# Optimization experiments

Hardware: AMD Instinct MI355X
Metric: run time of the kernel (lower is better)

The kernel has to match this reference:

```python
import jax, jax.numpy as jnp
import numpy as np

B, C, H, W = 8, 256, 64, 64
CI = 128  # inter_channels = in_channels // reduction

def _conv1x1(x, w, b):
    # x: [b, c, h, w], w: [o, c], b: [o]
    return jnp.einsum('bchw,oc->bohw', x, w) + b[None, :, None, None]

def setup_inputs() -> dict:
    key = jax.random.key(0)
    ks = jax.random.split(key, 5)
    s_in = 1.0 / np.sqrt(C)
    s_ci = 1.0 / np.sqrt(CI)
    return {
        'x': jax.random.normal(ks[0], (B, C, H, W), jnp.float32),
        'w_g': jax.random.normal(ks[1], (CI, C), jnp.float32) * s_in,
        'b_g': jnp.zeros((CI,), jnp.float32),
        'w_theta': jax.random.normal(ks[2], (CI, C), jnp.float32) * s_in,
        'b_theta': jnp.zeros((CI,), jnp.float32),
        'w_phi': jax.random.normal(ks[3], (CI, C), jnp.float32) * s_in,
        'b_phi': jnp.zeros((CI,), jnp.float32),
        'w_out': jax.random.normal(ks[4], (C, CI), jnp.float32) * s_ci,
        'b_out': jnp.zeros((C,), jnp.float32),
    }

def reference(x, w_g, b_g, w_theta, b_theta, w_phi, b_phi, w_out, b_out):
    n, c, h, w = x.shape
    N = h * w
    g_x = _conv1x1(x, w_g, b_g).reshape(n, CI, N).transpose(0, 2, 1)        # [b, N, ci]
    theta_x = _conv1x1(x, w_theta, b_theta).reshape(n, CI, N).transpose(0, 2, 1)  # [b, N, ci]
    phi_x = _conv1x1(x, w_phi, b_phi).reshape(n, CI, N)                     # [b, ci, N]
    pw = jnp.einsum('bnc,bcm->bnm', theta_x, phi_x)                         # [b, N, N]
    # Faithful to source: divides by ci**(-0.5) == multiplies by sqrt(ci)
    pw = pw / (jnp.asarray(CI, x.dtype) ** -0.5)
    pw = jax.nn.softmax(pw, axis=-1)
    y = jnp.einsum('bnm,bmc->bnc', pw, g_x)                                 # [b, N, ci]
    y = y.transpose(0, 2, 1).reshape(n, CI, h, w)
    return x + _conv1x1(y, w_out, b_out)
```

## Files before the change

kernel.cpp:

```cpp
#include <hip/hip_runtime.h>
#include <hip/hip_bf16.h>
#include <stdint.h>
#include <stddef.h>


typedef __bf16 bf16;
typedef __attribute__((ext_vector_type(8))) __bf16 bf16x8;
typedef __attribute__((ext_vector_type(4))) __bf16 bf16x4;
typedef __attribute__((ext_vector_type(4))) float  f32x4;
typedef __attribute__((ext_vector_type(4))) int    i32x4;

#define MFMA16(a, b, c) __builtin_amdgcn_mfma_f32_16x16x32_bf16((a), (b), (c), 0, 0, 0)

constexpr int NB  = 8;
constexpr int NC  = 256;
constexpr int NN  = 4096;
constexpr int NCI = 128;
constexpr size_t NEL = (size_t)NB * NN * NCI;
constexpr int PBATCH = NN * NCI;

#define QSCALE (11.313708498984761f * 1.4426950408889634f)


__global__ __launch_bounds__(256) void k_proj3(
    const float* __restrict__ x,
    const float* __restrict__ wt, const float* __restrict__ bt,
    const float* __restrict__ wp, const float* __restrict__ bp,
    const float* __restrict__ wg, const float* __restrict__ bg,
    const float* __restrict__ wo, bf16* __restrict__ wob,
    bf16* __restrict__ qh, bf16* __restrict__ ql,
    bf16* __restrict__ kh, bf16* __restrict__ kl,
    bf16* __restrict__ vv)
{
    const int nt  = blockIdx.x;
    const int b   = blockIdx.y;
    const int tid = threadIdx.x;
    const int wv  = tid >> 6;
    const int ln  = tid & 63;
    const int lg  = ln >> 4;
    const int lq  = ln & 15;

    if (wob != nullptr && tid < 16) {
        int idx = (b * 64 + nt) * 64 + tid * 4;
        f32x4 w4 = *(const f32x4*)(wo + idx);
        bf16x4 o4;
#pragma unroll
        for (int e = 0; e < 4; ++e) o4[e] = (bf16)w4[e];
        *(bf16x4*)(wob + idx) = o4;
    }

    __shared__ char lds[49152];
    char* Ah = lds;
    char* Al = lds + 8192;
    char* Wh = lds + 16384;
    char* Wl = lds + 32768;

    f32x4 acc[3][8];
#pragma unroll
    for (int pj = 0; pj < 3; ++pj)
#pragma unroll
        for (int j = 0; j < 8; ++j) acc[pj][j] = f32x4{0.f, 0.f, 0.f, 0.f};

    const int n0 = nt * 64;

    for (int c0 = 0; c0 < NC; c0 += 64) {
        __syncthreads();
#pragma unroll
        for (int p = 0; p < 4; ++p) {
            int cc = p * 16 + (tid >> 4);
            int nn = (tid & 15) * 4;
            f32x4 xv = *(const f32x4*)(x + ((size_t)b * NC + (c0 + cc)) * NN + n0 + nn);
#pragma unroll
            for (int e = 0; e < 4; ++e) {
                float f = xv[e];
                bf16 hh = (bf16)f;
                int row = nn + e;
                int off = (row * 128 + cc * 2) ^ ((row & 7) << 4);
                *(bf16*)(Ah + off) = hh;
                *(bf16*)(Al + off) = (bf16)(f - (float)hh);
            }
        }

#pragma unroll
        for (int pj = 0; pj < 3; ++pj) {
            const float* W = (pj == 0) ? wt : (pj == 1) ? wp : wg;
            const bool split = (pj != 2);
            if (pj != 0) __syncthreads();
#pragma unroll
            for (int p = 0; p < 8; ++p) {
                int i  = p * 16 + (tid >> 4);
                int c4 = (tid & 15) * 4;
                f32x4 w4 = *(const f32x4*)(W + (size_t)i * NC + c0 + c4);
                bf16x4 hv, lv;
#pragma unroll
                for (int e = 0; e < 4; ++e) {
                    bf16 hh = (bf16)w4[e];
                    hv[e] = hh;
                    lv[e] = (bf16)(w4[e] - (float)hh);
                }
                int off = (i * 128 + c4 * 2) ^ ((i & 7) << 4);
                *(bf16x4*)(Wh + off) = hv;
                if (split) *(bf16x4*)(Wl + off) = lv;
            }
            __syncthreads();
#pragma unroll
            for (int kk = 0; kk < 2; ++kk) {
                int row  = wv * 16 + lq;
                int koff = kk * 64 + lg * 16;
                int aoff = (row * 128 + koff) ^ ((row & 7) << 4);
                bf16x8 ah = *(const bf16x8*)(Ah + aoff);
                bf16x8 al = *(const bf16x8*)(Al + aoff);
#pragma unroll
                for (int j = 0; j < 8; ++j) {
                    int ir   = j * 16 + lq;
                    int woff = (ir * 128 + koff) ^ ((ir & 7) << 4);
                    bf16x8 bh = *(const bf16x8*)(Wh + woff);
                    acc[pj][j] = MFMA16(ah, bh, acc[pj][j]);
                    if (split) {
                        bf16x8 bl = *(const bf16x8*)(Wl + woff);
                        acc[pj][j] = MFMA16(ah, bl, acc[pj][j]);
                        acc[pj][j] = MFMA16(al, bh, acc[pj][j]);
                    }
                }
            }
        }
    }

#pragma unroll
    for (int j = 0; j < 8; ++j) {
        int i = j * 16 + lq;
        float bvt = bt[i];
        float bvp = bp[i];
#pragma unroll
        for (int r = 0; r < 4; ++r) {
            int q = n0 + wv * 16 + lg * 4 + r;
            size_t off = ((size_t)b * NN + q) * NCI + i;
            float vt2 = (acc[0][j][r] + bvt) * QSCALE;
            bf16 th = (bf16)vt2;
            qh[off] = th; ql[off] = (bf16)(vt2 - (float)th);
            float vp2 = acc[1][j][r] + bvp;
            bf16 phh = (bf16)vp2;
            kh[off] = phh; kl[off] = (bf16)(vp2 - (float)phh);
        }
    }

    __syncthreads();
    char* T = lds;
#pragma unroll
    for (int j = 0; j < 8; ++j) {
        int i = j * 16 + lq;
        float bv2 = bg[i];
#pragma unroll
        for (int r = 0; r < 4; ++r) {
            int nl = wv * 16 + lg * 4 + r;
            int off = (i * 128 + nl * 2) ^ ((i & 7) << 4);
            *(bf16*)(T + off) = (bf16)(acc[2][j][r] + bv2);
        }
    }
    __syncthreads();
#pragma unroll
    for (int p = 0; p < 4; ++p) {
        int i  = p * 32 + (tid >> 3);
        int sl = tid & 7;
        i32x4 tv = *(const i32x4*)(T + ((i * 128 + sl * 16) ^ ((i & 7) << 4)));
        size_t off = (size_t)b * PBATCH
                   + (size_t)((((nt * 8 + (i >> 4)) * 2 + (sl >> 2)) * 64
                               + (sl & 3) * 16 + (i & 15)) * 8);
        *(i32x4*)(vv + off) = tv;
    }
}

__global__ __launch_bounds__(128, 2) void k_attn_sp(
    const bf16* __restrict__ qh, const bf16* __restrict__ ql,
    const bf16* __restrict__ kh, const bf16* __restrict__ kl,
    const bf16* __restrict__ vf,
    bf16* __restrict__ p0, bf16* __restrict__ p1, float* __restrict__ ml)
{
    const int bid = blockIdx.x;
    const int b   = bid & 7;
    const int rs  = bid >> 3;
    const int qt  = rs & 63;
    const int h   = rs >> 6;
    const int tid = threadIdx.x;
    const int wv  = tid >> 6;
    const int ln  = tid & 63;
    const int lg  = ln >> 4;
    const int lq  = ln & 15;
    const int n0  = qt * 64;
    const int mb0 = h * 2048;
    bf16* ph = h ? p1 : p0;

    __shared__ __attribute__((aligned(16))) char lds[36864];
    char* P = lds + 32768 + wv * 2048;

    const int smm = tid >> 4;
    const int ssl = tid & 15;

    bf16x8 qhf[2][4], qlf[2][4];
#pragma unroll
    for (int q2 = 0; q2 < 2; ++q2) {
        int qrow = n0 + wv * 32 + q2 * 16 + lq;
        const bf16* bh = qh + ((size_t)b * NN + qrow) * NCI;
        const bf16* bl = ql + ((size_t)b * NN + qrow) * NCI;
#pragma unroll
        for (int kk = 0; kk < 4; ++kk) {
            qhf[q2][kk] = *(const bf16x8*)(bh + kk * 32 + lg * 8);
            qlf[q2][kk] = *(const bf16x8*)(bl + kk * 32 + lg * 8);
        }
    }

    f32x4 o[2][8];
#pragma unroll
    for (int q2 = 0; q2 < 2; ++q2)
#pragma unroll
        for (int j = 0; j < 8; ++j) o[q2][j] = f32x4{0.f, 0.f, 0.f, 0.f};
    float mrun[2] = {-1e30f, -1e30f};
    float lrun[2] = {0.f, 0.f};

    const bf16* vb = vf + (size_t)b * PBATCH + (size_t)ln * 8;

    {
#pragma unroll
        for (int p = 0; p < 4; ++p) {
            int mm = p * 8 + smm;
            size_t g = ((size_t)b * NN + mb0 + mm) * NCI + ssl * 8;
            i32x4 hv = *(const i32x4*)(kh + g);
            i32x4 lv = *(const i32x4*)(kl + g);
            int off = (mm * 256 + ssl * 16) ^ ((mm & 7) << 4);
            *(i32x4*)(lds + off) = hv;
            *(i32x4*)(lds + 8192 + off) = lv;
        }
    }
    __syncthreads();

    for (int t = 0; t < 64; ++t) {
        const int cur = t & 1;
        char* KHc = lds + cur * 16384;
        char* KLc = KHc + 8192;
        char* KHn = lds + (cur ^ 1) * 16384;
        char* KLn = KHn + 8192;
        const bool pre = (t < 63);

        i32x4 rkh[4], rkl[4];
        if (pre) {
#pragma unroll
            for (int p = 0; p < 4; ++p) {
                size_t g = ((size_t)b * NN + mb0 + (t + 1) * 32 + p * 8 + smm) * NCI + ssl * 8;
                rkh[p] = *(const i32x4*)(kh + g);
                rkl[p] = *(const i32x4*)(kl + g);
            }
        }
        __builtin_amdgcn_sched_barrier(0);

        f32x4 s[2][2];
        __builtin_amdgcn_s_setprio(1);
#pragma unroll
        for (int jm = 0; jm < 2; ++jm) {
            s[jm][0] = f32x4{0.f, 0.f, 0.f, 0.f};
            s[jm][1] = f32x4{0.f, 0.f, 0.f, 0.f};
            const int mrow = jm * 16 + lq;
            const int sw = (mrow & 7) << 4;
#pragma unroll
            for (int kk = 0; kk < 4; ++kk) {
                int aoff = (mrow * 256 + kk * 64 + lg * 16) ^ sw;
                bf16x8 ah = *(const bf16x8*)(KHc + aoff);
                bf16x8 al = *(const bf16x8*)(KLc + aoff);
                s[jm][0] = MFMA16(ah, qhf[0][kk], s[jm][0]);
                s[jm][1] = MFMA16(ah, qhf[1][kk], s[jm][1]);
                s[jm][0] = MFMA16(al, qhf[0][kk], s[jm][0]);
                s[jm][1] = MFMA16(al, qhf[1][kk], s[jm][1]);
                s[jm][0] = MFMA16(ah, qlf[0][kk], s[jm][0]);
                s[jm][1] = MFMA16(ah, qlf[1][kk], s[jm][1]);
            }
        }
        __builtin_amdgcn_s_setprio(0);

        bf16x8 bv[8];
        {
            const bf16* vp = vb + (size_t)(h * 32 + (t >> 1)) * 8192;
#pragma unroll
            for (int j = 0; j < 8; ++j)
                bv[j] = *(const bf16x8*)(vp + (j * 2 + (t & 1)) * 512);
        }
        __builtin_amdgcn_sched_barrier(0);

        if (pre) {
#pragma unroll
            for (int p = 0; p < 4; ++p) {
                int mm = p * 8 + smm;
                int off = (mm * 256 + ssl * 16) ^ ((mm & 7) << 4);
                *(i32x4*)(KHn + off) = rkh[p];
                *(i32x4*)(KLn + off) = rkl[p];
            }
        }

        float tm[2];
        tm[0] = s[0][0][0];
        tm[1] = s[0][1][0];
#pragma unroll
        for (int jm = 0; jm < 2; ++jm)
#pragma unroll
            for (int r = 0; r < 4; ++r) {
                tm[0] = fmaxf(tm[0], s[jm][0][r]);
                tm[1] = fmaxf(tm[1], s[jm][1][r]);
            }
#pragma unroll
        for (int q2 = 0; q2 < 2; ++q2) {
            tm[q2] = fmaxf(tm[q2], __shfl_xor(tm[q2], 16));
            tm[q2] = fmaxf(tm[q2], __shfl_xor(tm[q2], 32));
        }

        bool grow = (tm[0] > mrun[0] + 8.f) || (tm[1] > mrun[1] + 8.f);
        if (__any(grow)) {
            float alpha[2];
#pragma unroll
            for (int q2 = 0; q2 < 2; ++q2) {
                float mnew = fmaxf(mrun[q2], tm[q2]);
                alpha[q2] = exp2f(mrun[q2] - mnew);
                mrun[q2] = mnew;
                lrun[q2] *= alpha[q2];
            }
            float av0[4], av1[4];
#pragma unroll
            for (int r = 0; r < 4; ++r) {
                av0[r] = __shfl(alpha[0], lg * 4 + r);
                av1[r] = __shfl(alpha[1], lg * 4 + r);
            }
#pragma unroll
            for (int j = 0; j < 8; ++j)
#pragma unroll
                for (int r = 0; r < 4; ++r) {
                    o[0][j][r] *= av0[r];
                    o[1][j][r] *= av1[r];
                }
        }

        float psum[2] = {0.f, 0.f};
#pragma unroll
        for (int jm = 0; jm < 2; ++jm)
#pragma unroll
            for (int q2 = 0; q2 < 2; ++q2) {
                bf16x4 pk;
#pragma unroll
                for (int r = 0; r < 4; ++r) {
                    float e2 = exp2f(s[jm][q2][r] - mrun[q2]);
                    psum[q2] += e2;
                    pk[r] = (bf16)e2;
                }
                int row = q2 * 16 + lq;
                int off = (row * 64 + (jm * 16 + lg * 4) * 2) ^ ((row & 7) << 4);
                *(bf16x4*)(P + off) = pk;
            }
#pragma unroll
        for (int q2 = 0; q2 < 2; ++q2) {
            psum[q2] += __shfl_xor(psum[q2], 16);
            psum[q2] += __shfl_xor(psum[q2], 32);
            lrun[q2] += psum[q2];
        }

        bf16x8 pa[2];
#pragma unroll
        for (int q2 = 0; q2 < 2; ++q2) {
            int row = q2 * 16 + lq;
            pa[q2] = *(const bf16x8*)(P + ((row * 64 + lg * 16) ^ ((row & 7) << 4)));
        }
        __builtin_amdgcn_s_setprio(1);
#pragma unroll
        for (int j = 0; j < 8; ++j) {
            o[0][j] = MFMA16(pa[0], bv[j], o[0][j]);
            o[1][j] = MFMA16(pa[1], bv[j], o[1][j]);
        }
        __builtin_amdgcn_s_setprio(0);

        __syncthreads();
    }

    float rl0[4], rl1[4];
#pragma unroll
    for (int r = 0; r < 4; ++r) {
        rl0[r] = 1.f / __shfl(lrun[0], lg * 4 + r);
        rl1[r] = 1.f / __shfl(lrun[1], lg * 4 + r);
    }
#pragma unroll
    for (int j = 0; j < 8; ++j) {
        int d = j * 16 + lq;
#pragma unroll
        for (int r = 0; r < 4; ++r) {
            int q0 = n0 + wv * 32 + lg * 4 + r;
            ph[((size_t)b * NN + q0) * NCI + d]      = (bf16)(o[0][j][r] * rl0[r]);
            ph[((size_t)b * NN + q0 + 16) * NCI + d] = (bf16)(o[1][j][r] * rl1[r]);
        }
    }
    if (lg == 0) {
#pragma unroll
        for (int q2 = 0; q2 < 2; ++q2) {
            int row = n0 + wv * 32 + q2 * 16 + lq;
            size_t base = ((size_t)b * NN + row) * 4 + h * 2;
            ml[base]     = mrun[q2];
            ml[base + 1] = lrun[q2];
        }
    }
}

__global__ __launch_bounds__(256) void k_out(
    const bf16* __restrict__ p0, const bf16* __restrict__ p1,
    const float* __restrict__ ml, const float* __restrict__ x,
    const float* __restrict__ w_out, const bf16* __restrict__ wob,
    const float* __restrict__ b_out, float* __restrict__ out)
{
    const int nt  = blockIdx.x;
    const int b   = blockIdx.y;
    const int tid = threadIdx.x;
    const int wv  = tid >> 6;
    const int ln  = tid & 63;
    const int lg  = ln >> 4;
    const int lq  = ln & 15;
    const int n0  = nt * 64;

    __shared__ char Y[16384];
#pragma unroll
    for (int p = 0; p < 4; ++p) {
        int nn = p * 16 + (tid >> 4);
        int d0 = (tid & 15) * 8;
        size_t row = (size_t)b * NN + n0 + nn;
        f32x4 q = *(const f32x4*)(ml + row * 4);
        float M  = fmaxf(q[0], q[2]);
        float w0 = exp2f(q[0] - M) * q[1];
        float w1 = exp2f(q[2] - M) * q[3];
        float inv = 1.f / (w0 + w1);
        w0 *= inv; w1 *= inv;
        size_t off = row * NCI + d0;
        bf16x8 a = *(const bf16x8*)(p0 + off);
        bf16x8 c = *(const bf16x8*)(p1 + off);
        bf16x8 rr;
#pragma unroll
        for (int e = 0; e < 8; ++e)
            rr[e] = (bf16)(w0 * (float)a[e] + w1 * (float)c[e]);
        *(bf16x8*)(Y + ((nn * 256 + d0 * 2) ^ ((nn & 7) << 4))) = rr;
    }
    __syncthreads();

    bf16x8 af[4];
    {
        int row = wv * 16 + lq;
#pragma unroll
        for (int kk = 0; kk < 4; ++kk) {
            int koff = kk * 64 + lg * 16;
            af[kk] = *(const bf16x8*)(Y + ((row * 256 + koff) ^ ((row & 7) << 4)));
        }
    }

    f32x4 acc[16];
#pragma unroll
    for (int j = 0; j < 16; ++j) acc[j] = f32x4{0.f, 0.f, 0.f, 0.f};

    if (wob != nullptr) {
#pragma unroll
        for (int j = 0; j < 16; ++j) {
            int c = j * 16 + lq;
#pragma unroll
            for (int kk = 0; kk < 4; ++kk) {
                int i0 = kk * 32 + lg * 8;
                bf16x8 bw = *(const bf16x8*)(wob + (size_t)c * NCI + i0);
                acc[j] = MFMA16(af[kk], bw, acc[j]);
            }
        }
    } else {
#pragma unroll
        for (int j = 0; j < 16; ++j) {
            int c = j * 16 + lq;
#pragma unroll
            for (int kk = 0; kk < 4; ++kk) {
                int i0 = kk * 32 + lg * 8;
                f32x4 wa = *(const f32x4*)(w_out + (size_t)c * NCI + i0);
                f32x4 wb = *(const f32x4*)(w_out + (size_t)c * NCI + i0 + 4);
                bf16x8 bw;
#pragma unroll
                for (int e = 0; e < 4; ++e) { bw[e] = (bf16)wa[e]; bw[e + 4] = (bf16)wb[e]; }
                acc[j] = MFMA16(af[kk], bw, acc[j]);
            }
        }
    }

#pragma unroll
    for (int j = 0; j < 16; ++j) {
        int c = j * 16 + lq;
        int nb = n0 + wv * 16 + lg * 4;
        size_t off = ((size_t)b * NC + c) * (size_t)NN + nb;
        f32x4 xv = *(const f32x4*)(x + off);
        float bo = b_out[c];
        f32x4 r;
#pragma unroll
        for (int t = 0; t < 4; ++t) r[t] = acc[j][t] + xv[t] + bo;
        *(f32x4*)(out + off) = r;
    }
}

extern "C" void kernel_launch(void* const* d_in, const int* in_sizes, int n_in,
                              void* d_out, int out_size, void* d_ws, size_t ws_size,
                              hipStream_t stream)
{
    (void)in_sizes; (void)n_in; (void)out_size;
    const float* x  = (const float*)d_in[0];
    const float* wg = (const float*)d_in[1];
    const float* bg = (const float*)d_in[2];
    const float* wt = (const float*)d_in[3];
    const float* bt = (const float*)d_in[4];
    const float* wp = (const float*)d_in[5];
    const float* bp = (const float*)d_in[6];
    const float* wo = (const float*)d_in[7];
    const float* bo = (const float*)d_in[8];
    float* out = (float*)d_out;

    char* ws = (char*)d_ws;
    bf16* qh = (bf16*)(ws);
    bf16* ql = (bf16*)(ws + NEL * 2);
    bf16* kh = (bf16*)(ws + NEL * 4);
    bf16* kl = (bf16*)(ws + NEL * 6);
    bf16* vv = (bf16*)(ws + NEL * 8);
    bf16* p0 = (bf16*)(ws + NEL * 10);
    bf16* p1 = (bf16*)(ws + NEL * 12);
    float* ml = (float*)(ws + NEL * 14);
    const size_t ml_bytes = (size_t)NB * NN * 4 * sizeof(float);
    bf16* wob = nullptr;
    if (ws_size >= NEL * 14 + ml_bytes + (size_t)NC * NCI * sizeof(bf16))
        wob = (bf16*)(ws + NEL * 14 + ml_bytes);

    k_proj3<<<dim3(64, 8), 256, 0, stream>>>(x, wt, bt, wp, bp, wg, bg,
                                             wo, wob, qh, ql, kh, kl, vv);
    k_attn_sp<<<dim3(1024), 128, 0, stream>>>(qh, ql, kh, kl, vv, p0, p1, ml);
    k_out<<<dim3(64, 8), 256, 0, stream>>>(p0, p1, ml, x, wo, wob, bo, out);
}
```

Before: 236.0 us.

## Stream K tiles into LDS via direct global_load_lds with pre-swizzled K layout

The projection kernel now writes the split-bf16 K tensors in a tiled, pre-swizzled layout, one contiguous 32-row block per tile. The attention kernel then double-buffers K tiles using global_load_lds 16-byte direct-to-LDS loads instead of loading into registers and storing to LDS. This frees VGPRs and removes the LDS write instructions from the main loop, at the cost of coupling the K layout between the two kernels. It also relies on the existing barrier to cover completion of the asynchronous LDS fills.

Result: no change. 236.6 us (+0.3%).

```diff
diff --git a/kernel.cpp b/kernel.cpp
--- a/kernel.cpp
+++ b/kernel.cpp
@@ -11,6 +11,12 @@
 typedef __attribute__((ext_vector_type(4))) int    i32x4;
 
 #define MFMA16(a, b, c) __builtin_amdgcn_mfma_f32_16x16x32_bf16((a), (b), (c), 0, 0, 0)
+
+__device__ __forceinline__ void gload_lds16(const void* g, void* l) {
+    __builtin_amdgcn_global_load_lds(
+        (const __attribute__((address_space(1))) void*)g,
+        (__attribute__((address_space(3))) void*)l, 16, 0, 0);
+}
 
 constexpr int NB  = 8;
 constexpr int NC  = 256;
@@ -140,7 +146,9 @@
             qh[off] = th; ql[off] = (bf16)(vt2 - (float)th);
             float vp2 = acc[1][j][r] + bvp;
             bf16 phh = (bf16)vp2;
-            kh[off] = phh; kl[off] = (bf16)(vp2 - (float)phh);
+            size_t ko = (size_t)b * PBATCH + (size_t)(q >> 5) * 4096
+                      + (size_t)((q & 31) * 128 + (((i >> 3) ^ (q & 7)) << 3) + (i & 7));
+            kh[ko] = phh; kl[ko] = (bf16)(vp2 - (float)phh);
         }
     }
 
@@ -172,7 +180,7 @@
 
 __global__ __launch_bounds__(128, 2) void k_attn_sp(
     const bf16* __restrict__ qh, const bf16* __restrict__ ql,
-    const bf16* __restrict__ kh, const bf16* __restrict__ kl,
+    const bf16* __restrict__ khp, const bf16* __restrict__ klp,
     const bf16* __restrict__ vf,
     bf16* __restrict__ p0, bf16* __restrict__ p1, float* __restrict__ ml)
 {
@@ -187,14 +195,13 @@
     const int lg  = ln >> 4;
     const int lq  = ln & 15;
     const int n0  = qt * 64;
-    const int mb0 = h * 2048;
     bf16* ph = h ? p1 : p0;
 
     __shared__ __attribute__((aligned(16))) char lds[36864];
     char* P = lds + 32768 + wv * 2048;
 
-    const int smm = tid >> 4;
-    const int ssl = tid & 15;
+    const bf16* ksh = khp + (size_t)b * PBATCH + wv * 2048 + (size_t)ln * 8;
+    const bf16* ksl = klp + (size_t)b * PBATCH + wv * 2048 + (size_t)ln * 8;
 
     bf16x8 qhf[2][4], qlf[2][4];
 #pragma unroll
@@ -220,15 +227,14 @@
     const bf16* vb = vf + (size_t)b * PBATCH + (size_t)ln * 8;
 
     {
-#pragma unroll
-        for (int p = 0; p < 4; ++p) {
-            int mm = p * 8 + smm;
-            size_t g = ((size_t)b * NN + mb0 + mm) * NCI + ssl * 8;
-            i32x4 hv = *(const i32x4*)(kh + g);
-            i32x4 lv = *(const i32x4*)(kl + g);
-            int off = (mm * 256 + ssl * 16) ^ ((mm & 7) << 4);
-            *(i32x4*)(lds + off) = hv;
-            *(i32x4*)(lds + 8192 + off) = lv;
+        const bf16* sh = ksh + (size_t)(h * 64) * 4096;
+        const bf16* sl = ksl + (size_t)(h * 64) * 4096;
+        char* dh = lds + wv * 4096;
+        char* dl = lds + 8192 + wv * 4096;
+#pragma unroll
+        for (int c = 0; c < 4; ++c) {
+            gload_lds16(sh + c * 512, dh + c * 1024);
+            gload_lds16(sl + c * 512, dl + c * 1024);
         }
     }
     __syncthreads();
@@ -241,13 +247,15 @@
         char* KLn = KHn + 8192;
         const bool pre = (t < 63);
 
-        i32x4 rkh[4], rkl[4];
         if (pre) {
-#pragma unroll
-            for (int p = 0; p < 4; ++p) {
-                size_t g = ((size_t)b * NN + mb0 + (t + 1) * 32 + p * 8 + smm) * NCI + ssl * 8;
-                rkh[p] = *(const i32x4*)(kh + g);
-                rkl[p] = *(const i32x4*)(kl + g);
+            const bf16* sh = ksh + (size_t)(h * 64 + t + 1) * 4096;
+            const bf16* sl = ksl + (size_t)(h * 64 + t + 1) * 4096;
+            char* dh = KHn + wv * 4096;
+            char* dl = KLn + wv * 4096;
+#pragma unroll
+            for (int c = 0; c < 4; ++c) {
+                gload_lds16(sh + c * 512, dh + c * 1024);
+                gload_lds16(sl + c * 512, dl + c * 1024);
             }
         }
         __builtin_amdgcn_sched_barrier(0);
@@ -283,16 +291,6 @@
                 bv[j] = *(const bf16x8*)(vp + (j * 2 + (t & 1)) * 512);
         }
         __builtin_amdgcn_sched_barrier(0);
-
-        if (pre) {
-#pragma unroll
-            for (int p = 0; p < 4; ++p) {
-                int mm = p * 8 + smm;
-                int off = (mm * 256 + ssl * 16) ^ ((mm & 7) << 4);
-                *(i32x4*)(KHn + off) = rkh[p];
-                *(i32x4*)(KLn + off) = rkl[p];
-            }
-        }
 
         float tm[2];
         tm[0] = s[0][0][0];
```
